# Kernel tuning notes

Measured on AMD Instinct MI355X. Metric: run time of the kernel, lower is better.

Reference implementation:

```python
import jax, jax.numpy as jnp
import numpy as np

B, S, D, H = 2, 2048, 1024, 16
DH = D // H
EPS = 1e-5
NEG = -1e9


def layer_norm(x, scale, bias):
    mu = jnp.mean(x, axis=-1, keepdims=True)
    var = jnp.mean((x - mu) ** 2, axis=-1, keepdims=True)
    return (x - mu) * jax.lax.rsqrt(var + EPS) * scale + bias


def setup_inputs() -> dict:
    key = jax.random.key(0)
    ks = jax.random.split(key, 8)
    scale = 1.0 / np.sqrt(D)
    x = jax.random.normal(ks[0], (B, S, D), dtype=jnp.float32)
    padding_mask = jnp.ones((B, S), dtype=bool)
    # per-head QKV projections stacked over heads: (H, D, DH)
    Wq = jax.random.normal(ks[1], (H, D, DH), dtype=jnp.float32) * scale
    Wk = jax.random.normal(ks[2], (H, D, DH), dtype=jnp.float32) * scale
    Wv = jax.random.normal(ks[3], (H, D, DH), dtype=jnp.float32) * scale
    ln1_s = jnp.ones((D,), jnp.float32); ln1_b = jnp.zeros((D,), jnp.float32)
    ln2_s = jnp.ones((D,), jnp.float32); ln2_b = jnp.zeros((D,), jnp.float32)
    W1 = jax.random.normal(ks[4], (D, D), dtype=jnp.float32) * scale
    b1 = jnp.zeros((D,), jnp.float32)
    W2 = jax.random.normal(ks[5], (D, D), dtype=jnp.float32) * scale
    b2 = jnp.zeros((D,), jnp.float32)
    return dict(x=x, padding_mask=padding_mask, Wq=Wq, Wk=Wk, Wv=Wv,
                ln1_s=ln1_s, ln1_b=ln1_b, ln2_s=ln2_s, ln2_b=ln2_b,
                W1=W1, b1=b1, W2=W2, b2=b2)


def reference(x, padding_mask, Wq, Wk, Wv, ln1_s, ln1_b, ln2_s, ln2_b, W1, b1, W2, b2):
    # pre-norm attention with residual (dropout = identity at eval)
    h = layer_norm(x, ln1_s, ln1_b)
    q = jnp.einsum('bsd,hde->bhse', h, Wq)
    k = jnp.einsum('bsd,hde->bhse', h, Wk)
    v = jnp.einsum('bsd,hde->bhse', h, Wv)
    scores = jnp.einsum('bhse,bhte->bhst', q, k) / jnp.sqrt(jnp.float32(DH))
    causal = jnp.tril(jnp.ones((S, S), dtype=bool))           # (S,S)
    mask = padding_mask[:, None, None, :] & causal[None, None]  # (B,1,S,S)
    scores = jnp.where(mask, scores, NEG)
    p = jax.nn.softmax(scores, axis=-1)
    z = jnp.einsum('bhst,bhte->bshe', p, v).reshape(x.shape[0], x.shape[1], D)
    x = x + z
    # pre-norm FFN with residual
    h2 = layer_norm(x, ln2_s, ln2_b)
    ff = jax.nn.relu(h2 @ W1 + b1) @ W2 + b2
    return x + ff
```

## Files before the change

### kernel.cpp

```cpp
#include <hip/hip_runtime.h>
#include <hip/hip_bf16.h>
#include <stdint.h>

#define NB 2
#define NS 2048
#define ND 1024
#define NH 16
#define NDH 64
#define NT (NB*NS)

using f32x4  = __attribute__((ext_vector_type(4))) float;
using bf16x8 = __attribute__((ext_vector_type(8))) short;

typedef __attribute__((address_space(1))) unsigned int as1_uint;
typedef __attribute__((address_space(3))) unsigned int as3_uint;

#if __has_builtin(__builtin_amdgcn_exp2f)
#define EXP2 __builtin_amdgcn_exp2f
#else
#define EXP2 exp2f
#endif

__device__ __forceinline__ void llds16(void* l, const void* g) {
    __builtin_amdgcn_global_load_lds((as1_uint*)g, (as3_uint*)l, 16, 0, 0);
}

__device__ __forceinline__ f32x4 mfma16(bf16x8 a, bf16x8 b, f32x4 c) {
    return __builtin_amdgcn_mfma_f32_16x16x32_bf16(a, b, c, 0, 0, 0);
}

__device__ __forceinline__ unsigned short f2bf(float f) {
    union { __hip_bfloat16 h; unsigned short u; } cv;
    cv.h = __float2bfloat16(f);
    return cv.u;
}

__global__ void k_prep_ln(const float* __restrict__ Wq, const float* __restrict__ Wk,
                          const float* __restrict__ Wv, const float* __restrict__ W1,
                          const float* __restrict__ W2, unsigned short* __restrict__ WcatT,
                          unsigned short* __restrict__ W1T, unsigned short* __restrict__ W2T,
                          const float* __restrict__ x, const float* __restrict__ sc,
                          const float* __restrict__ bi, unsigned short* __restrict__ hout) {
    __shared__ float tile[64][65];
    __shared__ float ssum[4], ssq[4];
    int tid = threadIdx.x;
    int bid = blockIdx.x;
    if (bid < 768) {
        const float SCALEQ = 0.125f * 1.44269504088896f;
        int kt = bid & 15; bid >>= 4;
        int h  = bid & 15; bid >>= 4;
        int mat = bid;
        const float* W = (mat == 0) ? Wq : (mat == 1) ? Wk : Wv;
#pragma unroll
        for (int i = 0; i < 16; ++i) {
            int idx = tid + i * 256;
            int r = idx >> 6, e = idx & 63;
            tile[r][e] = W[(size_t)h * ND * NDH + (size_t)(kt * 64 + r) * NDH + e];
        }
        __syncthreads();
#pragma unroll
        for (int i = 0; i < 16; ++i) {
            int idx = tid + i * 256;
            int e = idx >> 6, r = idx & 63;
            float v = tile[r][e];
            if (mat == 0) v *= SCALEQ;
            WcatT[(size_t)(mat * 1024 + h * 64 + e) * ND + kt * 64 + r] = f2bf(v);
        }
    } else if (bid < 1280) {
        const float* W = (bid < 1024) ? W1 : W2;
        unsigned short* WT = (bid < 1024) ? W1T : W2T;
        int lb = (bid - 768) & 255;
        int ntile = lb & 15;
        int ktile = lb >> 4;
#pragma unroll
        for (int i = 0; i < 16; ++i) {
            int idx = tid + i * 256;
            int r = idx >> 6, c = idx & 63;
            tile[r][c] = W[(size_t)(ktile * 64 + r) * ND + ntile * 64 + c];
        }
        __syncthreads();
#pragma unroll
        for (int i = 0; i < 16; ++i) {
            int idx = tid + i * 256;
            int c = idx >> 6, r = idx & 63;
            WT[(size_t)(ntile * 64 + c) * ND + ktile * 64 + r] = f2bf(tile[r][c]);
        }
    } else {
        int row = bid - 1280;
        const float* xr = x + (size_t)row * ND;
        float4 v = reinterpret_cast<const float4*>(xr)[tid];
        float sum = v.x + v.y + v.z + v.w;
        float sq  = v.x * v.x + v.y * v.y + v.z * v.z + v.w * v.w;
#pragma unroll
        for (int off = 1; off < 64; off <<= 1) {
            sum += __shfl_xor(sum, off);
            sq  += __shfl_xor(sq, off);
        }
        int wave = tid >> 6;
        if ((tid & 63) == 0) { ssum[wave] = sum; ssq[wave] = sq; }
        __syncthreads();
        sum = ssum[0] + ssum[1] + ssum[2] + ssum[3];
        sq  = ssq[0] + ssq[1] + ssq[2] + ssq[3];
        float mu  = sum * (1.0f / ND);
        float var = sq * (1.0f / ND) - mu * mu;
        float rstd = rsqrtf(var + 1e-5f);
        float4 s4 = reinterpret_cast<const float4*>(sc)[tid];
        float4 b4 = reinterpret_cast<const float4*>(bi)[tid];
        ushort4 o;
        o.x = f2bf((v.x - mu) * rstd * s4.x + b4.x);
        o.y = f2bf((v.y - mu) * rstd * s4.y + b4.y);
        o.z = f2bf((v.z - mu) * rstd * s4.z + b4.z);
        o.w = f2bf((v.w - mu) * rstd * s4.w + b4.w);
        reinterpret_cast<ushort4*>(hout + (size_t)row * ND)[tid] = o;
    }
}

__global__ void k_ln(const float* __restrict__ x, const float* __restrict__ sc,
                     const float* __restrict__ bi, unsigned short* __restrict__ out) {
    int row = blockIdx.x;
    int tid = threadIdx.x;
    const float* xr = x + (size_t)row * ND;
    float4 v = reinterpret_cast<const float4*>(xr)[tid];
    float sum = v.x + v.y + v.z + v.w;
    float sq  = v.x * v.x + v.y * v.y + v.z * v.z + v.w * v.w;
#pragma unroll
    for (int off = 1; off < 64; off <<= 1) {
        sum += __shfl_xor(sum, off);
        sq  += __shfl_xor(sq, off);
    }
    __shared__ float ssum[4], ssq[4];
    int wave = tid >> 6;
    if ((tid & 63) == 0) { ssum[wave] = sum; ssq[wave] = sq; }
    __syncthreads();
    sum = ssum[0] + ssum[1] + ssum[2] + ssum[3];
    sq  = ssq[0] + ssq[1] + ssq[2] + ssq[3];
    float mu  = sum * (1.0f / ND);
    float var = sq * (1.0f / ND) - mu * mu;
    float rstd = rsqrtf(var + 1e-5f);
    float4 s4 = reinterpret_cast<const float4*>(sc)[tid];
    float4 b4 = reinterpret_cast<const float4*>(bi)[tid];
    ushort4 o;
    o.x = f2bf((v.x - mu) * rstd * s4.x + b4.x);
    o.y = f2bf((v.y - mu) * rstd * s4.y + b4.y);
    o.z = f2bf((v.z - mu) * rstd * s4.z + b4.z);
    o.w = f2bf((v.w - mu) * rstd * s4.w + b4.w);
    reinterpret_cast<ushort4*>(out + (size_t)row * ND)[tid] = o;
}

template<bool BIAS, bool RELU, bool RES>
__device__ __forceinline__
void gemm_core(const unsigned short* __restrict__ A, const unsigned short* __restrict__ Bt,
               const float* __restrict__ bias, const float* __restrict__ res,
               void* __restrict__ Cv, int N, int K, int wg) {
    __shared__ __align__(16) unsigned short As[2][64 * 64];
    __shared__ __align__(16) unsigned short Bs[2][128 * 64];
    int tid = threadIdx.x;
    int lane = tid & 63, wave = tid >> 6;
    int wm = wave >> 1, wn = wave & 1;
    int l16 = lane & 15, lg = lane >> 4;
    int ntiles = N >> 7;
    int mt = wg / ntiles;
    int nt = wg % ntiles;

    int srow = tid >> 3;
    int sch  = tid & 7;
    int scs  = sch ^ (srow & 7);
    int KT = K >> 6;

    const unsigned short* Asrc = A  + (size_t)(mt * 64 + srow) * K + scs * 8;
    const unsigned short* Bsrc = Bt + (size_t)(nt * 128 + srow) * K + scs * 8;

    f32x4 acc[2][4];
#pragma unroll
    for (int i = 0; i < 2; ++i)
#pragma unroll
        for (int j = 0; j < 4; ++j) acc[i][j] = (f32x4){0.f, 0.f, 0.f, 0.f};

    auto STAGE = [&](int kt, int bufi) {
        const unsigned short* a = Asrc + kt * 64;
        const unsigned short* b = Bsrc + kt * 64;
        char* ad = (char*)As[bufi] + wave * 1024;
        char* bd = (char*)Bs[bufi] + wave * 1024;
        llds16(ad,         a);
        llds16(ad + 4096,  a + (size_t)32 * K);
        llds16(bd,         b);
        llds16(bd + 4096,  b + (size_t)32 * K);
        llds16(bd + 8192,  b + (size_t)64 * K);
        llds16(bd + 12288, b + (size_t)96 * K);
    };

    auto COMPUTE = [&](int cb) {
        bf16x8 af[2][2], bfb[4][2];
#pragma unroll
        for (int mi = 0; mi < 2; ++mi)
#pragma unroll
            for (int kc = 0; kc < 2; ++kc) {
                int row = wm * 32 + mi * 16 + l16;
                int ch = (kc * 4 + lg) ^ (row & 7);
                af[mi][kc] = *reinterpret_cast<const bf16x8*>((const char*)As[cb] + row * 128 + ch * 16);
            }
#pragma unroll
        for (int ni = 0; ni < 4; ++ni)
#pragma unroll
            for (int kc = 0; kc < 2; ++kc) {
                int row = wn * 64 + ni * 16 + l16;
                int ch = (kc * 4 + lg) ^ (row & 7);
                bfb[ni][kc] = *reinterpret_cast<const bf16x8*>((const char*)Bs[cb] + row * 128 + ch * 16);
            }
#pragma unroll
        for (int mi = 0; mi < 2; ++mi)
#pragma unroll
            for (int ni = 0; ni < 4; ++ni) {
                acc[mi][ni] = mfma16(af[mi][0], bfb[ni][0], acc[mi][ni]);
                acc[mi][ni] = mfma16(af[mi][1], bfb[ni][1], acc[mi][ni]);
            }
    };

    STAGE(0, 0);
    for (int kt = 0; kt < KT; kt += 2) {
        STAGE(kt + 1, 1);
        asm volatile("s_waitcnt vmcnt(6)" ::: "memory");
        __builtin_amdgcn_s_barrier();
        COMPUTE(0);
        __builtin_amdgcn_s_barrier();
        if (kt + 2 < KT) {
            STAGE(kt + 2, 0);
            asm volatile("s_waitcnt vmcnt(6)" ::: "memory");
        } else {
            asm volatile("s_waitcnt vmcnt(0)" ::: "memory");
        }
        __builtin_amdgcn_s_barrier();
        COMPUTE(1);
        __builtin_amdgcn_s_barrier();
    }

#pragma unroll
    for (int mi = 0; mi < 2; ++mi)
#pragma unroll
        for (int ni = 0; ni < 4; ++ni) {
            int col = nt * 128 + wn * 64 + ni * 16 + l16;
            float bv = BIAS ? bias[col] : 0.f;
#pragma unroll
            for (int r = 0; r < 4; ++r) {
                int row = mt * 64 + wm * 32 + mi * 16 + lg * 4 + r;
                float v = acc[mi][ni][r] + bv;
                if (RELU) v = fmaxf(v, 0.f);
                size_t idx = (size_t)row * N + col;
                if (RES) ((float*)Cv)[idx] = v + res[idx];
                else ((unsigned short*)Cv)[idx] = f2bf(v);
            }
        }
}

template<bool BIAS, bool RELU, bool RES>
__device__ __forceinline__
void gemm_core128(const unsigned short* __restrict__ A, const unsigned short* __restrict__ Bt,
                  const float* __restrict__ bias, const float* __restrict__ res,
                  void* __restrict__ Cv, int N, int K, int wg) {
    __shared__ __align__(16) unsigned short As[2][128 * 64];
    __shared__ __align__(16) unsigned short Bs[2][128 * 64];
    int tid = threadIdx.x;
    int lane = tid & 63, wave = tid >> 6;
    int wm = wave >> 1, wn = wave & 1;
    int l16 = lane & 15, lg = lane >> 4;
    int ntiles = N >> 7;
    int mt = wg / ntiles;
    int nt = wg % ntiles;

    int srow = tid >> 3;
    int sch  = tid & 7;
    int scs  = sch ^ (srow & 7);
    int KT = K >> 6;

    const unsigned short* Asrc = A  + (size_t)(mt * 128 + srow) * K + scs * 8;
    const unsigned short* Bsrc = Bt + (size_t)(nt * 128 + srow) * K + scs * 8;

    f32x4 acc[4][4];
#pragma unroll
    for (int i = 0; i < 4; ++i)
#pragma unroll
        for (int j = 0; j < 4; ++j) acc[i][j] = (f32x4){0.f, 0.f, 0.f, 0.f};

    auto STAGE = [&](int kt, int bufi) {
        const unsigned short* a = Asrc + kt * 64;
        const unsigned short* b = Bsrc + kt * 64;
        char* ad = (char*)As[bufi] + wave * 1024;
        char* bd = (char*)Bs[bufi] + wave * 1024;
        llds16(ad,         a);
        llds16(ad + 4096,  a + (size_t)32 * K);
        llds16(ad + 8192,  a + (size_t)64 * K);
        llds16(ad + 12288, a + (size_t)96 * K);
        llds16(bd,         b);
        llds16(bd + 4096,  b + (size_t)32 * K);
        llds16(bd + 8192,  b + (size_t)64 * K);
        llds16(bd + 12288, b + (size_t)96 * K);
    };

    auto COMPUTE = [&](int cb) {
        bf16x8 af[4][2], bfb[4][2];
#pragma unroll
        for (int mi = 0; mi < 4; ++mi)
#pragma unroll
            for (int kc = 0; kc < 2; ++kc) {
                int row = wm * 64 + mi * 16 + l16;
                int ch = (kc * 4 + lg) ^ (row & 7);
                af[mi][kc] = *reinterpret_cast<const bf16x8*>((const char*)As[cb] + row * 128 + ch * 16);
            }
#pragma unroll
        for (int ni = 0; ni < 4; ++ni)
#pragma unroll
            for (int kc = 0; kc < 2; ++kc) {
                int row = wn * 64 + ni * 16 + l16;
                int ch = (kc * 4 + lg) ^ (row & 7);
                bfb[ni][kc] = *reinterpret_cast<const bf16x8*>((const char*)Bs[cb] + row * 128 + ch * 16);
            }
#pragma unroll
        for (int mi = 0; mi < 4; ++mi)
#pragma unroll
            for (int ni = 0; ni < 4; ++ni) {
                acc[mi][ni] = mfma16(af[mi][0], bfb[ni][0], acc[mi][ni]);
                acc[mi][ni] = mfma16(af[mi][1], bfb[ni][1], acc[mi][ni]);
            }
    };

    STAGE(0, 0);
    for (int kt = 0; kt < KT; kt += 2) {
        STAGE(kt + 1, 1);
        asm volatile("s_waitcnt vmcnt(8)" ::: "memory");
        __builtin_amdgcn_s_barrier();
        COMPUTE(0);
        __builtin_amdgcn_s_barrier();
        if (kt + 2 < KT) {
            STAGE(kt + 2, 0);
            asm volatile("s_waitcnt vmcnt(8)" ::: "memory");
        } else {
            asm volatile("s_waitcnt vmcnt(0)" ::: "memory");
        }
        __builtin_amdgcn_s_barrier();
        COMPUTE(1);
        __builtin_amdgcn_s_barrier();
    }

#pragma unroll
    for (int mi = 0; mi < 4; ++mi)
#pragma unroll
        for (int ni = 0; ni < 4; ++ni) {
            int col = nt * 128 + wn * 64 + ni * 16 + l16;
            float bv = BIAS ? bias[col] : 0.f;
#pragma unroll
            for (int r = 0; r < 4; ++r) {
                int row = mt * 128 + wm * 64 + mi * 16 + lg * 4 + r;
                float v = acc[mi][ni][r] + bv;
                if (RELU) v = fmaxf(v, 0.f);
                size_t idx = (size_t)row * N + col;
                if (RES) ((float*)Cv)[idx] = v + res[idx];
                else ((unsigned short*)Cv)[idx] = f2bf(v);
            }
        }
}

template<bool BIAS, bool RELU, bool RES>
__global__ __launch_bounds__(256)
void k_gemm(const unsigned short* __restrict__ A, const unsigned short* __restrict__ Bt,
            const float* __restrict__ bias, const float* __restrict__ res,
            void* __restrict__ Cv, int N, int K) {
    int wg = (blockIdx.x & 7) * (gridDim.x >> 3) + (blockIdx.x >> 3);
    gemm_core<BIAS, RELU, RES>(A, Bt, bias, res, Cv, N, K, wg);
}

__global__ __launch_bounds__(256)
void k_gemm_dual(const unsigned short* __restrict__ A0, const unsigned short* __restrict__ Bt0,
                 void* __restrict__ C0, int N0,
                 const unsigned short* __restrict__ A1, const unsigned short* __restrict__ Bt1,
                 void* __restrict__ C1, int N1, int K, int split) {
    int bid = blockIdx.x;
    if (bid < split) {
        int wg = (bid & 7) * (split >> 3) + (bid >> 3);
        gemm_core128<false, false, false>(A0, Bt0, nullptr, nullptr, C0, N0, K, wg);
    } else {
        int lb = bid - split;
        int nblk = gridDim.x - split;
        int wg = (lb & 7) * (nblk >> 3) + (lb >> 3);
        gemm_core128<false, false, false>(A1, Bt1, nullptr, nullptr, C1, N1, K, wg);
    }
}

__global__ __launch_bounds__(256)
void k_attn(const unsigned short* __restrict__ qk, const unsigned short* __restrict__ VT,
            const float* __restrict__ x, float* __restrict__ x2) {
    constexpr int ldq = 2 * ND;
    int bid = blockIdx.x;
    int c  = bid & 255;
    int g  = bid >> 8;
    int s  = c >> 5;
    int bh = c & 31;
    int qb = (g == 0) ? 31 - s : (g == 1) ? 16 + s : (g == 2) ? 15 - s : s;
    int h = bh & 15, b = bh >> 4;
    int tid = threadIdx.x;
    int lane = tid & 63, wave = tid >> 6;
    int l16 = lane & 15, lg = lane >> 4;

    const unsigned short* Qp = qk + (size_t)b * NS * ldq + h * NDH;
    const unsigned short* Kp = Qp + ND;
    const unsigned short* Vp = VT + (size_t)(h * NDH) * NT + b * NS;

    __shared__ __align__(16) unsigned short Ks[2][64 * 64];
    __shared__ __align__(16) unsigned short Vs[2][64 * 64];
    __shared__ __align__(16) unsigned short Ps[4][16 * 64];

    int srow = tid >> 3;
    int sch  = tid & 7;
    int scs  = sch ^ (srow & 7);

    int nt = qb + 1;
    int qw = qb * 64 + wave * 16;

    const unsigned short* Kn = Kp + (size_t)srow * ldq + scs * 8;
    const unsigned short* Vn = Vp + (size_t)srow * NT + scs * 8;

    bf16x8 qf[2];
#pragma unroll
    for (int kc = 0; kc < 2; ++kc)
        qf[kc] = *reinterpret_cast<const bf16x8*>(Qp + (size_t)(qw + l16) * ldq + kc * 32 + lg * 8);

    bf16x8 vone;
#pragma unroll
    for (int i = 0; i < 8; ++i) vone[i] = (short)0x3F80;

    f32x4 oacc[4];
#pragma unroll
    for (int i = 0; i < 4; ++i) oacc[i] = (f32x4){0.f, 0.f, 0.f, 0.f};
    f32x4 lacc = (f32x4){0.f, 0.f, 0.f, 0.f};

    char* pbase = (char*)&Ps[wave][0] + l16 * 128;
    int psw = l16 & 7;

    llds16((char*)Ks[0] + wave * 1024,        Kn);
    llds16((char*)Ks[0] + wave * 1024 + 4096, Kn + (size_t)32 * ldq);
    llds16((char*)Vs[0] + wave * 1024,        Vn);
    llds16((char*)Vs[0] + wave * 1024 + 4096, Vn + (size_t)32 * NT);
    Kn += (size_t)64 * ldq;
    Vn += 64;

    auto BODY = [&](int t, int cur) {
        if (t + 1 < nt) {
            char* kd = (char*)Ks[cur ^ 1] + wave * 1024;
            char* vd = (char*)Vs[cur ^ 1] + wave * 1024;
            llds16(kd,        Kn);
            llds16(kd + 4096, Kn + (size_t)32 * ldq);
            llds16(vd,        Vn);
            llds16(vd + 4096, Vn + (size_t)32 * NT);
            Kn += (size_t)64 * ldq;
            Vn += 64;
            asm volatile("s_waitcnt vmcnt(4)" ::: "memory");
        } else {
            asm volatile("s_waitcnt vmcnt(0)" ::: "memory");
        }
        __builtin_amdgcn_s_barrier();

        f32x4 st[4];
#pragma unroll
        for (int mtt = 0; mtt < 4; ++mtt) st[mtt] = (f32x4){0.f, 0.f, 0.f, 0.f};
        __builtin_amdgcn_s_setprio(1);
#pragma unroll
        for (int kc = 0; kc < 2; ++kc)
#pragma unroll
            for (int mtt = 0; mtt < 4; ++mtt) {
                int row = mtt * 16 + l16;
                int ch = (kc * 4 + lg) ^ (row & 7);
                bf16x8 kf = *reinterpret_cast<const bf16x8*>((const char*)Ks[cur] + row * 128 + ch * 16);
                st[mtt] = mfma16(kf, qf[kc], st[mtt]);
            }
        __builtin_amdgcn_s_setprio(0);

        if (t == qb) {
            int qg = qw + l16;
#pragma unroll
            for (int mtt = 0; mtt < 4; ++mtt)
#pragma unroll
                for (int r = 0; r < 4; ++r) {
                    int key = t * 64 + mtt * 16 + lg * 4 + r;
                    st[mtt][r] = (key <= qg) ? st[mtt][r] : -1.0e30f;
                }
        }
#pragma unroll
        for (int mtt = 0; mtt < 4; ++mtt) {
            float p0 = EXP2(st[mtt][0]);
            float p1 = EXP2(st[mtt][1]);
            float p2 = EXP2(st[mtt][2]);
            float p3 = EXP2(st[mtt][3]);
            int b0 = mtt * 32 + lg * 8;
            int sb = ((((b0 >> 4) ^ psw) << 4) | (b0 & 15));
            uint2 u;
            u.x = (unsigned)f2bf(p0) | ((unsigned)f2bf(p1) << 16);
            u.y = (unsigned)f2bf(p2) | ((unsigned)f2bf(p3) << 16);
            *reinterpret_cast<uint2*>(pbase + sb) = u;
        }

        asm volatile("s_waitcnt lgkmcnt(0)" ::: "memory");

        __builtin_amdgcn_s_setprio(1);
#pragma unroll
        for (int kc = 0; kc < 2; ++kc) {
            bf16x8 pa = *reinterpret_cast<const bf16x8*>(pbase + (((kc * 4 + lg) ^ psw) << 4));
            lacc = mfma16(pa, vone, lacc);
#pragma unroll
            for (int ntt = 0; ntt < 4; ++ntt) {
                int vrow = ntt * 16 + l16;
                bf16x8 vb = *reinterpret_cast<const bf16x8*>(
                    (const char*)Vs[cur] + vrow * 128 + ((((kc * 4 + lg) ^ (vrow & 7)) << 4)));
                oacc[ntt] = mfma16(pa, vb, oacc[ntt]);
            }
        }
        __builtin_amdgcn_s_setprio(0);
        __builtin_amdgcn_s_barrier();
    };

    for (int t = 0; t < nt; t += 2) {
        BODY(t, 0);
        if (t + 1 < nt) BODY(t + 1, 1);
    }

#pragma unroll
    for (int r = 0; r < 4; ++r) {
        float linv = 1.0f / lacc[r];
        int tkn = b * NS + qw + lg * 4 + r;
        size_t base = (size_t)tkn * ND + h * NDH;
#pragma unroll
        for (int ntt = 0; ntt < 4; ++ntt) {
            size_t idx = base + ntt * 16 + l16;
            x2[idx] = x[idx] + oacc[ntt][r] * linv;
        }
    }
}

extern "C" void kernel_launch(void* const* d_in, const int* in_sizes, int n_in,
                              void* d_out, int out_size, void* d_ws, size_t ws_size,
                              hipStream_t stream) {
    const float* x    = (const float*)d_in[0];
    const float* Wq   = (const float*)d_in[2];
    const float* Wk   = (const float*)d_in[3];
    const float* Wv   = (const float*)d_in[4];
    const float* ln1s = (const float*)d_in[5];
    const float* ln1b = (const float*)d_in[6];
    const float* ln2s = (const float*)d_in[7];
    const float* ln2b = (const float*)d_in[8];
    const float* W1   = (const float*)d_in[9];
    const float* b1   = (const float*)d_in[10];
    const float* W2   = (const float*)d_in[11];
    const float* b2   = (const float*)d_in[12];
    float* out = (float*)d_out;

    char* ws = (char*)d_ws;
    unsigned short* WcatT = (unsigned short*)(ws);
    unsigned short* W1T   = (unsigned short*)(ws + 6291456);
    unsigned short* W2T   = (unsigned short*)(ws + 8388608);
    unsigned short* hbuf  = (unsigned short*)(ws + 10485760);
    unsigned short* qkbuf = (unsigned short*)(ws + 18874368);
    unsigned short* vtbuf = (unsigned short*)(ws + 35651584);
    float*          x2    = (float*)(ws + 44040192);
    unsigned short* ubuf  = qkbuf;

    k_prep_ln<<<1280 + NT, 256, 0, stream>>>(Wq, Wk, Wv, W1, W2, WcatT, W1T, W2T,
                                             x, ln1s, ln1b, hbuf);
    k_gemm_dual<<<512 + 256, 256, 0, stream>>>(
        hbuf, WcatT, qkbuf, 2048,
        WcatT + (size_t)2048 * 1024, hbuf, vtbuf, NT, 1024, 512);
    k_attn<<<NB * NH * 32, 256, 0, stream>>>(qkbuf, vtbuf, x, x2);
    k_ln<<<NT, 256, 0, stream>>>(x2, ln2s, ln2b, hbuf);
    k_gemm<true, true, false><<<(NT / 64) * (1024 / 128), 256, 0, stream>>>(
        hbuf, W1T, b1, nullptr, ubuf, 1024, 1024);
    k_gemm<true, false, true><<<(NT / 64) * (1024 / 128), 256, 0, stream>>>(
        ubuf, W2T, b2, x2, out, 1024, 1024);
}
```

Before: 124.1 us.

## Double attention query tile per block to 128 rows, reusing K/V tiles

Each attention block now handles 128 query rows instead of 64, and each wave computes two 16-row query sub-tiles that share every K and V fragment loaded from LDS. The grid halves to 512 blocks with a new heavy/light ordering of query tiles. This halves K/V global loads and LDS reads per query row, at the cost of more registers, a larger P scratch buffer, fewer blocks in flight, and masking applied over a wider diagonal region.

```diff
diff --git a/kernel.cpp b/kernel.cpp
--- a/kernel.cpp
+++ b/kernel.cpp
@@ -390,11 +390,10 @@
             const float* __restrict__ x, float* __restrict__ x2) {
     constexpr int ldq = 2 * ND;
     int bid = blockIdx.x;
-    int c  = bid & 255;
+    int bh = bid & 31;
+    int s  = (bid >> 5) & 7;
     int g  = bid >> 8;
-    int s  = c >> 5;
-    int bh = c & 31;
-    int qb = (g == 0) ? 31 - s : (g == 1) ? 16 + s : (g == 2) ? 15 - s : s;
+    int qt = g ? s : 15 - s;
     int h = bh & 15, b = bh >> 4;
     int tid = threadIdx.x;
     int lane = tid & 63, wave = tid >> 6;
@@ -406,33 +405,36 @@
 
     __shared__ __align__(16) unsigned short Ks[2][64 * 64];
     __shared__ __align__(16) unsigned short Vs[2][64 * 64];
-    __shared__ __align__(16) unsigned short Ps[4][16 * 64];
+    __shared__ __align__(16) unsigned short Ps[8][16 * 64];
 
     int srow = tid >> 3;
     int sch  = tid & 7;
     int scs  = sch ^ (srow & 7);
 
-    int nt = qb + 1;
-    int qw = qb * 64 + wave * 16;
+    int nt = 2 * qt + 2;
+    int qw = qt * 128 + wave * 32;
 
     const unsigned short* Kn = Kp + (size_t)srow * ldq + scs * 8;
     const unsigned short* Vn = Vp + (size_t)srow * NT + scs * 8;
 
-    bf16x8 qf[2];
-#pragma unroll
-    for (int kc = 0; kc < 2; ++kc)
-        qf[kc] = *reinterpret_cast<const bf16x8*>(Qp + (size_t)(qw + l16) * ldq + kc * 32 + lg * 8);
+    bf16x8 qfA[2], qfB[2];
+#pragma unroll
+    for (int kc = 0; kc < 2; ++kc) {
+        qfA[kc] = *reinterpret_cast<const bf16x8*>(Qp + (size_t)(qw + l16) * ldq + kc * 32 + lg * 8);
+        qfB[kc] = *reinterpret_cast<const bf16x8*>(Qp + (size_t)(qw + 16 + l16) * ldq + kc * 32 + lg * 8);
+    }
 
     bf16x8 vone;
 #pragma unroll
     for (int i = 0; i < 8; ++i) vone[i] = (short)0x3F80;
 
-    f32x4 oacc[4];
-#pragma unroll
-    for (int i = 0; i < 4; ++i) oacc[i] = (f32x4){0.f, 0.f, 0.f, 0.f};
-    f32x4 lacc = (f32x4){0.f, 0.f, 0.f, 0.f};
-
-    char* pbase = (char*)&Ps[wave][0] + l16 * 128;
+    f32x4 oA[4], oB[4];
+#pragma unroll
+    for (int i = 0; i < 4; ++i) { oA[i] = (f32x4){0.f,0.f,0.f,0.f}; oB[i] = (f32x4){0.f,0.f,0.f,0.f}; }
+    f32x4 lA = (f32x4){0.f,0.f,0.f,0.f}, lB = (f32x4){0.f,0.f,0.f,0.f};
+
+    char* pbA = (char*)&Ps[wave * 2 + 0][0] + l16 * 128;
+    char* pbB = (char*)&Ps[wave * 2 + 1][0] + l16 * 128;
     int psw = l16 & 7;
 
     llds16((char*)Ks[0] + wave * 1024,        Kn);
@@ -458,9 +460,9 @@
         }
         __builtin_amdgcn_s_barrier();
 
-        f32x4 st[4];
-#pragma unroll
-        for (int mtt = 0; mtt < 4; ++mtt) st[mtt] = (f32x4){0.f, 0.f, 0.f, 0.f};
+        f32x4 stA[4], stB[4];
+#pragma unroll
+        for (int mtt = 0; mtt < 4; ++mtt) { stA[mtt] = (f32x4){0.f,0.f,0.f,0.f}; stB[mtt] = (f32x4){0.f,0.f,0.f,0.f}; }
         __builtin_amdgcn_s_setprio(1);
 #pragma unroll
         for (int kc = 0; kc < 2; ++kc)
@@ -469,32 +471,33 @@
                 int row = mtt * 16 + l16;
                 int ch = (kc * 4 + lg) ^ (row & 7);
                 bf16x8 kf = *reinterpret_cast<const bf16x8*>((const char*)Ks[cur] + row * 128 + ch * 16);
-                st[mtt] = mfma16(kf, qf[kc], st[mtt]);
+                stA[mtt] = mfma16(kf, qfA[kc], stA[mtt]);
+                stB[mtt] = mfma16(kf, qfB[kc], stB[mtt]);
             }
         __builtin_amdgcn_s_setprio(0);
 
-        if (t == qb) {
-            int qg = qw + l16;
+        if (64 * t + 63 > qw) {
+            int qA = qw + l16, qB = qw + 16 + l16;
 #pragma unroll
             for (int mtt = 0; mtt < 4; ++mtt)
 #pragma unroll
                 for (int r = 0; r < 4; ++r) {
                     int key = t * 64 + mtt * 16 + lg * 4 + r;
-                    st[mtt][r] = (key <= qg) ? st[mtt][r] : -1.0e30f;
+                    stA[mtt][r] = (key <= qA) ? stA[mtt][r] : -1.0e30f;
+                    stB[mtt][r] = (key <= qB) ? stB[mtt][r] : -1.0e30f;
                 }
         }
 #pragma unroll
         for (int mtt = 0; mtt < 4; ++mtt) {
-            float p0 = EXP2(st[mtt][0]);
-            float p1 = EXP2(st[mtt][1]);
-            float p2 = EXP2(st[mtt][2]);
-            float p3 = EXP2(st[mtt][3]);
             int b0 = mtt * 32 + lg * 8;
             int sb = ((((b0 >> 4) ^ psw) << 4) | (b0 & 15));
-            uint2 u;
-            u.x = (unsigned)f2bf(p0) | ((unsigned)f2bf(p1) << 16);
-            u.y = (unsigned)f2bf(p2) | ((unsigned)f2bf(p3) << 16);
-            *reinterpret_cast<uint2*>(pbase + sb) = u;
+            uint2 uA, uB;
+            uA.x = (unsigned)f2bf(EXP2(stA[mtt][0])) | ((unsigned)f2bf(EXP2(stA[mtt][1])) << 16);
+            uA.y = (unsigned)f2bf(EXP2(stA[mtt][2])) | ((unsigned)f2bf(EXP2(stA[mtt][3])) << 16);
+            uB.x = (unsigned)f2bf(EXP2(stB[mtt][0])) | ((unsigned)f2bf(EXP2(stB[mtt][1])) << 16);
+            uB.y = (unsigned)f2bf(EXP2(stB[mtt][2])) | ((unsigned)f2bf(EXP2(stB[mtt][3])) << 16);
+            *reinterpret_cast<uint2*>(pbA + sb) = uA;
+            *reinterpret_cast<uint2*>(pbB + sb) = uB;
         }
 
         asm volatile("s_waitcnt lgkmcnt(0)" ::: "memory");
@@ -502,14 +505,17 @@
         __builtin_amdgcn_s_setprio(1);
 #pragma unroll
         for (int kc = 0; kc < 2; ++kc) {
-            bf16x8 pa = *reinterpret_cast<const bf16x8*>(pbase + (((kc * 4 + lg) ^ psw) << 4));
-            lacc = mfma16(pa, vone, lacc);
+            bf16x8 paA = *reinterpret_cast<const bf16x8*>(pbA + (((kc * 4 + lg) ^ psw) << 4));
+            bf16x8 paB = *reinterpret_cast<const bf16x8*>(pbB + (((kc * 4 + lg) ^ psw) << 4));
+            lA = mfma16(paA, vone, lA);
+            lB = mfma16(paB, vone, lB);
 #pragma unroll
             for (int ntt = 0; ntt < 4; ++ntt) {
                 int vrow = ntt * 16 + l16;
                 bf16x8 vb = *reinterpret_cast<const bf16x8*>(
                     (const char*)Vs[cur] + vrow * 128 + ((((kc * 4 + lg) ^ (vrow & 7)) << 4)));
-                oacc[ntt] = mfma16(pa, vb, oacc[ntt]);
+                oA[ntt] = mfma16(paA, vb, oA[ntt]);
+                oB[ntt] = mfma16(paB, vb, oB[ntt]);
             }
         }
         __builtin_amdgcn_s_setprio(0);
@@ -518,18 +524,23 @@
 
     for (int t = 0; t < nt; t += 2) {
         BODY(t, 0);
-        if (t + 1 < nt) BODY(t + 1, 1);
+        BODY(t + 1, 1);
     }
 
 #pragma unroll
     for (int r = 0; r < 4; ++r) {
-        float linv = 1.0f / lacc[r];
-        int tkn = b * NS + qw + lg * 4 + r;
-        size_t base = (size_t)tkn * ND + h * NDH;
+        float livA = 1.0f / lA[r];
+        float livB = 1.0f / lB[r];
+        int tknA = b * NS + qw + lg * 4 + r;
+        int tknB = tknA + 16;
+        size_t baseA = (size_t)tknA * ND + h * NDH;
+        size_t baseB = (size_t)tknB * ND + h * NDH;
 #pragma unroll
         for (int ntt = 0; ntt < 4; ++ntt) {
-            size_t idx = base + ntt * 16 + l16;
-            x2[idx] = x[idx] + oacc[ntt][r] * linv;
+            size_t iA = baseA + ntt * 16 + l16;
+            size_t iB = baseB + ntt * 16 + l16;
+            x2[iA] = x[iA] + oA[ntt][r] * livA;
+            x2[iB] = x[iB] + oB[ntt][r] * livB;
         }
     }
 }
@@ -566,7 +577,7 @@
     k_gemm_dual<<<512 + 256, 256, 0, stream>>>(
         hbuf, WcatT, qkbuf, 2048,
         WcatT + (size_t)2048 * 1024, hbuf, vtbuf, NT, 1024, 512);
-    k_attn<<<NB * NH * 32, 256, 0, stream>>>(qkbuf, vtbuf, x, x2);
+    k_attn<<<512, 256, 0, stream>>>(qkbuf, vtbuf, x, x2);
     k_ln<<<NT, 256, 0, stream>>>(x2, ln2s, ln2b, hbuf);
     k_gemm<true, true, false><<<(NT / 64) * (1024 / 128), 256, 0, stream>>>(
         hbuf, W1T, b1, nullptr, ubuf, 1024, 1024);
```

Result: slower. 134.4 us (+8.3%).
